# Optimization experiments

Hardware: AMD Instinct MI355X
Metric: run time of the kernel (lower is better)

The kernel has to match this reference:

```python
import jax, jax.numpy as jnp
import numpy as np

B, N, D = 16384, 32, 256
J, P = 23, 2  # num_joints, dim_per_out_node


def setup_inputs() -> dict:
    key = jax.random.key(0)
    k1, k2, k3 = jax.random.split(key, 3)
    x = jax.random.normal(k1, (B, N, D), dtype=jnp.float32)
    # per-joint Linear params: weight [J, P, D] (torch Linear layout), bias [J, P]
    W = jax.random.normal(k2, (J, P, D), dtype=jnp.float32) * (1.0 / np.sqrt(D))
    b = jax.random.normal(k3, (J, P), dtype=jnp.float32) * 0.01
    # node_for_joint[j] = index of the node mapped to joint j (here nodes 0..22)
    node_for_joint = jnp.arange(J, dtype=jnp.int32)
    return {"x": x, "W": W, "b": b, "node_for_joint": node_for_joint}


def reference(x, W, b, node_for_joint):
    # Gather the node embedding feeding each joint: [B, J, D]
    xj = x[:, node_for_joint, :]
    # Apply each joint's distinct tiny Linear head as one batched contraction.
    # out[b, j, p] = sum_d xj[b, j, d] * W[j, p, d] + b[j, p]
    out = jnp.einsum("bjd,jpd->bjp", xj, W) + b  # [B, J, P]
    return out
```

## Files before the change

kernel.cpp:

```cpp
#include <hip/hip_runtime.h>


constexpr int Bn = 16384;
constexpr int Nn = 32;
constexpr int Dn = 256;
constexpr int Jn = 23;
constexpr int Pn = 2;

__global__ __launch_bounds__(256) void detok_kernel(
    const float* __restrict__ x, const float* __restrict__ W,
    const float* __restrict__ bias, const int* __restrict__ nfj,
    float* __restrict__ out)
{
    const int tid   = blockIdx.x * blockDim.x + threadIdx.x;
    const int wave  = tid >> 6;
    const int lane  = threadIdx.x & 63;
    const int group = lane >> 4;
    const int gl    = lane & 15;

    const int pair = wave * 4 + group;
    const int b = pair / Jn;
    const int j = pair - b * Jn;
    const int node = nfj[j];

    const float4* __restrict__ xr =
        reinterpret_cast<const float4*>(x + ((size_t)b * Nn + node) * Dn);
    const float4* __restrict__ w0 =
        reinterpret_cast<const float4*>(W + ((size_t)j * Pn + 0) * Dn);
    const float4* __restrict__ w1 =
        reinterpret_cast<const float4*>(W + ((size_t)j * Pn + 1) * Dn);

    float s0 = 0.f, s1 = 0.f;
#pragma unroll
    for (int k = 0; k < 4; ++k) {
        const int idx = k * 16 + gl;
        float4 xv = xr[idx];
        float4 a0 = w0[idx];
        float4 a1 = w1[idx];
        s0 += xv.x * a0.x + xv.y * a0.y + xv.z * a0.z + xv.w * a0.w;
        s1 += xv.x * a1.x + xv.y * a1.y + xv.z * a1.z + xv.w * a1.w;
    }

#pragma unroll
    for (int off = 8; off >= 1; off >>= 1) {
        s0 += __shfl_xor(s0, off, 64);
        s1 += __shfl_xor(s1, off, 64);
    }

    if (gl == 0) {
        float2 bj = *reinterpret_cast<const float2*>(bias + j * Pn);
        float2 o;
        o.x = s0 + bj.x;
        o.y = s1 + bj.y;
        *reinterpret_cast<float2*>(out + (size_t)pair * Pn) = o;
    }
}

extern "C" void kernel_launch(void* const* d_in, const int* in_sizes, int n_in,
                              void* d_out, int out_size, void* d_ws, size_t ws_size,
                              hipStream_t stream) {
    const float* x    = (const float*)d_in[0];
    const float* W    = (const float*)d_in[1];
    const float* bias = (const float*)d_in[2];
    const int*   nfj  = (const int*)d_in[3];
    float* out = (float*)d_out;

    const int total_pairs = Bn * Jn;
    const int pairs_per_block = (256 / 64) * 4;
    const int grid = total_pairs / pairs_per_block;

    detok_kernel<<<grid, 256, 0, stream>>>(x, W, bias, nfj, out);
}
```

Baseline: 642.9 us.

## Tile batch rows per joint with 2D grid to reuse weights across rows

The kernel now uses a 2D grid with one joint per blockIdx.y, and each 16-lane group handles four batch rows for that joint. Each weight float4 load is reused for four dot products instead of one, and the per-pair division by the joint count is gone. The x traffic stays about the same, about 23*16384*1KB, so the kernel is likely still memory-bound. In exchange, the output writes are strided across batch rows, each wave issues more independent loads, and there are fewer total threads.

```diff
diff --git a/kernel.cpp b/kernel.cpp
--- a/kernel.cpp
+++ b/kernel.cpp
@@ -7,52 +7,78 @@
 constexpr int Jn = 23;
 constexpr int Pn = 2;
 
+__device__ __forceinline__ float dot4(float4 a, float4 b) {
+    return a.x * b.x + a.y * b.y + a.z * b.z + a.w * b.w;
+}
+
 __global__ __launch_bounds__(256) void detok_kernel(
     const float* __restrict__ x, const float* __restrict__ W,
     const float* __restrict__ bias, const int* __restrict__ nfj,
     float* __restrict__ out)
 {
-    const int tid   = blockIdx.x * blockDim.x + threadIdx.x;
-    const int wave  = tid >> 6;
-    const int lane  = threadIdx.x & 63;
-    const int group = lane >> 4;
-    const int gl    = lane & 15;
+    const int j    = blockIdx.y;
+    const int node = nfj[j];
+    const int lane = threadIdx.x & 63;
+    const int wid  = threadIdx.x >> 6;
+    const int grp  = lane >> 4;
+    const int gl   = lane & 15;
 
-    const int pair = wave * 4 + group;
-    const int b = pair / Jn;
-    const int j = pair - b * Jn;
-    const int node = nfj[j];
+    const int b0 = (blockIdx.x * 16 + wid * 4 + grp) * 4;
 
-    const float4* __restrict__ xr =
-        reinterpret_cast<const float4*>(x + ((size_t)b * Nn + node) * Dn);
     const float4* __restrict__ w0 =
         reinterpret_cast<const float4*>(W + ((size_t)j * Pn + 0) * Dn);
     const float4* __restrict__ w1 =
         reinterpret_cast<const float4*>(W + ((size_t)j * Pn + 1) * Dn);
 
-    float s0 = 0.f, s1 = 0.f;
+    const float4* __restrict__ xr0 =
+        reinterpret_cast<const float4*>(x + ((size_t)(b0 + 0) * Nn + node) * Dn);
+    const float4* __restrict__ xr1 =
+        reinterpret_cast<const float4*>(x + ((size_t)(b0 + 1) * Nn + node) * Dn);
+    const float4* __restrict__ xr2 =
+        reinterpret_cast<const float4*>(x + ((size_t)(b0 + 2) * Nn + node) * Dn);
+    const float4* __restrict__ xr3 =
+        reinterpret_cast<const float4*>(x + ((size_t)(b0 + 3) * Nn + node) * Dn);
+
+    float s00 = 0.f, s01 = 0.f, s10 = 0.f, s11 = 0.f;
+    float s20 = 0.f, s21 = 0.f, s30 = 0.f, s31 = 0.f;
+
 #pragma unroll
     for (int k = 0; k < 4; ++k) {
         const int idx = k * 16 + gl;
-        float4 xv = xr[idx];
         float4 a0 = w0[idx];
         float4 a1 = w1[idx];
-        s0 += xv.x * a0.x + xv.y * a0.y + xv.z * a0.z + xv.w * a0.w;
-        s1 += xv.x * a1.x + xv.y * a1.y + xv.z * a1.z + xv.w * a1.w;
+        float4 x0 = xr0[idx];
+        float4 x1 = xr1[idx];
+        float4 x2 = xr2[idx];
+        float4 x3 = xr3[idx];
+        s00 += dot4(x0, a0); s01 += dot4(x0, a1);
+        s10 += dot4(x1, a0); s11 += dot4(x1, a1);
+        s20 += dot4(x2, a0); s21 += dot4(x2, a1);
+        s30 += dot4(x3, a0); s31 += dot4(x3, a1);
     }
 
 #pragma unroll
     for (int off = 8; off >= 1; off >>= 1) {
-        s0 += __shfl_xor(s0, off, 64);
-        s1 += __shfl_xor(s1, off, 64);
+        s00 += __shfl_xor(s00, off, 64);
+        s01 += __shfl_xor(s01, off, 64);
+        s10 += __shfl_xor(s10, off, 64);
+        s11 += __shfl_xor(s11, off, 64);
+        s20 += __shfl_xor(s20, off, 64);
+        s21 += __shfl_xor(s21, off, 64);
+        s30 += __shfl_xor(s30, off, 64);
+        s31 += __shfl_xor(s31, off, 64);
     }
 
     if (gl == 0) {
-        float2 bj = *reinterpret_cast<const float2*>(bias + j * Pn);
-        float2 o;
-        o.x = s0 + bj.x;
-        o.y = s1 + bj.y;
-        *reinterpret_cast<float2*>(out + (size_t)pair * Pn) = o;
+        const float2 bj = *reinterpret_cast<const float2*>(bias + j * Pn);
+        float2 o0 = make_float2(s00 + bj.x, s01 + bj.y);
+        float2 o1 = make_float2(s10 + bj.x, s11 + bj.y);
+        float2 o2 = make_float2(s20 + bj.x, s21 + bj.y);
+        float2 o3 = make_float2(s30 + bj.x, s31 + bj.y);
+        *reinterpret_cast<float2*>(out + ((size_t)(b0 + 0) * Jn + j) * Pn) = o0;
+        *reinterpret_cast<float2*>(out + ((size_t)(b0 + 1) * Jn + j) * Pn) = o1;
+        *reinterpret_cast<float2*>(out + ((size_t)(b0 + 2) * Jn + j) * Pn) = o2;
+        *reinterpret_cast<float2*>(out + ((size_t)(b0 + 3) * Jn + j) * Pn) = o3;
     }
 }
 
@@ -65,9 +91,6 @@
     const int*   nfj  = (const int*)d_in[3];
     float* out = (float*)d_out;
 
-    const int total_pairs = Bn * Jn;
-    const int pairs_per_block = (256 / 64) * 4;
-    const int grid = total_pairs / pairs_per_block;
-
+    dim3 grid(Bn / 64, Jn);
     detok_kernel<<<grid, 256, 0, stream>>>(x, W, bias, nfj, out);
 }
```

After: 679.3 us. 5.7% more time.
